# Kernel tuning notes

Hardware: AMD Instinct MI355X
Metric: run time of the kernel (lower is better)

The kernel has to match this reference:

```python
import jax, jax.numpy as jnp
import numpy as np
import math

B, S, D, H = 4, 2048, 1024, 16
DK = D // H  # 64


def setup_inputs() -> dict:
    key = jax.random.key(0)
    ks = jax.random.split(key, 10)
    scale = 1.0 / math.sqrt(D)
    inp = {
        "context_sequence": jax.random.normal(ks[0], (B, S, D), dtype=jnp.float32),
        "value_sequence": jax.random.normal(ks[1], (B, S, D), dtype=jnp.float32),
        "mask": jax.random.randint(ks[2], (S, S), 0, 2, dtype=jnp.int32),
        # stacked per-head projection params: [H, D, DK] weights, [H, DK] biases
        "Wq": jax.random.uniform(ks[3], (H, D, DK), jnp.float32, -scale, scale),
        "bq": jnp.zeros((H, DK), jnp.float32),
        "Wk": jax.random.uniform(ks[4], (H, D, DK), jnp.float32, -scale, scale),
        "bk": jnp.zeros((H, DK), jnp.float32),
        "Wv": jax.random.uniform(ks[5], (H, D, DK), jnp.float32, -scale, scale),
        "bv": jnp.zeros((H, DK), jnp.float32),
        "Wo": jax.random.uniform(ks[6], (D, D), jnp.float32, -scale, scale),
        "bo": jnp.zeros((D,), jnp.float32),
    }
    return inp


def reference(context_sequence, value_sequence, mask, Wq, bq, Wk, bk, Wv, bv, Wo, bo):
    # per-head projections batched over heads: [B,H,S,DK]
    Q = jnp.einsum("bsd,hdk->bhsk", context_sequence, Wq) + bq[None, :, None, :]
    K = jnp.einsum("bsd,hdk->bhsk", context_sequence, Wk) + bk[None, :, None, :]
    V = jnp.einsum("bsd,hdk->bhsk", value_sequence, Wv) + bv[None, :, None, :]
    scores = jnp.einsum("bhsk,bhtk->bhst", Q, K) / math.sqrt(DK)
    scores = jnp.where(mask[None, None, :, :] == 1, jnp.float32(-1e9), scores)
    attn = jax.nn.softmax(scores, axis=-1)
    out = jnp.einsum("bhst,bhtk->bhsk", attn, V)  # [B,H,S,DK]
    concat = out.transpose(0, 2, 1, 3).reshape(B, S, D)  # heads concatenated
    # output projection (dropout is identity in eval mode)
    return concat @ Wo.T + bo
```

## Files before the change

### kernel.cpp

```cpp
#include <hip/hip_runtime.h>
#include <hip/hip_bf16.h>

#define DEVI __device__ __forceinline__

typedef __attribute__((ext_vector_type(8))) short bf16x8;
typedef __attribute__((ext_vector_type(4))) float f32x4;
typedef unsigned short u16;
typedef unsigned long long u64;


DEVI void async16(const void* g, const void* l) {
  __builtin_amdgcn_global_load_lds(
      (const __attribute__((address_space(1))) unsigned int*)g,
      (__attribute__((address_space(3))) unsigned int*)l, 16, 0, 0);
}

DEVI u16 f2bf(float x) {
  unsigned int u = __float_as_uint(x);
  return (u16)((u + 0x7fffu + ((u >> 16) & 1u)) >> 16);
}

DEVI float fast_exp2(float x) {
#if __has_builtin(__builtin_amdgcn_exp2f)
  return __builtin_amdgcn_exp2f(x);
#else
  return exp2f(x);
#endif
}


__global__ __launch_bounds__(256) void prep_kernel(
    const float* __restrict__ ctx, const float* __restrict__ val, const int* __restrict__ msk,
    const float* __restrict__ Wq, const float* __restrict__ Wk, const float* __restrict__ Wv,
    const float* __restrict__ Wo, const float* __restrict__ bq, const float* __restrict__ bk,
    u16* __restrict__ Xc, u16* __restrict__ Xv, u16* __restrict__ Wqt, u16* __restrict__ Wkt,
    u16* __restrict__ Wvt, u16* __restrict__ WoB, u64* __restrict__ mbits, float* __restrict__ bqk) {
  __shared__ float tile[64 * 69];
  const int blk = blockIdx.x, tid = threadIdx.x;
  if (blk < 16384) {
    const float* src = (blk < 8192) ? ctx : val;
    u16* dst = (blk < 8192) ? Xc : Xv;
    int i = (blk & 8191) * 256 + tid;
    float4 v = ((const float4*)src)[i];
    ushort4 o;
    o.x = f2bf(v.x); o.y = f2bf(v.y); o.z = f2bf(v.z); o.w = f2bf(v.w);
    ((ushort4*)dst)[i] = o;
  } else if (blk < 17408) {
    int i = (blk - 16384) * 256 + tid;
    float4 v = ((const float4*)Wo)[i];
    ushort4 o;
    o.x = f2bf(v.x); o.y = f2bf(v.y); o.z = f2bf(v.z); o.w = f2bf(v.w);
    ((ushort4*)WoB)[i] = o;
  } else if (blk < 18176) {
    int t = blk - 17408;
    int mat = t >> 8, r = t & 255, h = r >> 4, d0 = (r & 15) * 64;
    const float* Ws = (mat == 0) ? Wq : (mat == 1) ? Wk : Wv;
    u16* Wd = (mat == 0) ? Wqt : (mat == 1) ? Wkt : Wvt;
    const int dg = tid & 15, rg = tid >> 4;
#pragma unroll
    for (int i = 0; i < 4; i++) {
      int dr = rg + i * 16;
      float4 v = *(const float4*)&Ws[((size_t)(h * 1024 + d0 + dr)) * 64 + dg * 4];
      tile[dr * 69 + dg * 4 + 0] = v.x;
      tile[dr * 69 + dg * 4 + 1] = v.y;
      tile[dr * 69 + dg * 4 + 2] = v.z;
      tile[dr * 69 + dg * 4 + 3] = v.w;
    }
    __syncthreads();
#pragma unroll
    for (int i = 0; i < 4; i++) {
      int k = rg + i * 16;
      ushort4 o;
      o.x = f2bf(tile[(dg * 4 + 0) * 69 + k]);
      o.y = f2bf(tile[(dg * 4 + 1) * 69 + k]);
      o.z = f2bf(tile[(dg * 4 + 2) * 69 + k]);
      o.w = f2bf(tile[(dg * 4 + 3) * 69 + k]);
      *(ushort4*)&Wd[(size_t)(h * 64 + k) * 1024 + d0 + dg * 4] = o;
    }
  } else if (blk < 34560) {
    int gid = (blk - 18176) * 256 + tid;
    u64 bal = __ballot(msk[gid] == 1);
    if ((tid & 63) == 0) mbits[(size_t)((gid >> 6) & 31) * 2048 + (gid >> 11)] = bal;
  } else {
    int i = (blk - 34560) * 256 + tid;
    bqk[i] = (i < 1024) ? bq[i] : bk[i - 1024];
  }
}


__global__ __launch_bounds__(256) void qkv_gemm(const u16* __restrict__ Xc, const u16* __restrict__ Xv,
                                                const u16* __restrict__ Wqkt, const u16* __restrict__ Wvt,
                                                const float* __restrict__ bqk, const float* __restrict__ bvv,
                                                u16* __restrict__ QKb, u16* __restrict__ Vtg, float qscale) {
  __shared__ __align__(16) u16 As[128 * 32];
  __shared__ __align__(16) u16 Bs[128 * 32];
  const int tid = threadIdx.x;
  const int w = tid >> 6, lane = tid & 63, quad = lane >> 4, lc = lane & 15;
  const int K = 1024;
  const bool isV = blockIdx.y >= 16;
  const int m0 = blockIdx.x * 128;
  const int n0 = (isV ? (blockIdx.y - 16) : blockIdx.y) * 128;
  const u16* A  = isV ? Xv : Xc;
  const u16* Bt = isV ? Wvt : Wqkt;
  const float* bias = isV ? bvv : bqk;
  const int wrow = (w >> 1) * 64, wcol = (w & 1) * 64;
  const int srow = tid >> 2, sc = tid & 3;
  const u16* Ag = A + (size_t)(m0 + srow) * K + sc * 8;
  const u16* Bg = Bt + (size_t)(n0 + srow) * K + sc * 8;
  u16* Asw = As + w * 512;
  u16* Bsw = Bs + w * 512;

  f32x4 acc[4][4] = {};
  for (int k0 = 0; k0 < K; k0 += 32) {
    async16(Ag + k0, Asw);
    async16(Ag + k0 + (size_t)64 * K, Asw + 2048);
    async16(Bg + k0, Bsw);
    async16(Bg + k0 + (size_t)64 * K, Bsw + 2048);
    __syncthreads();
    bf16x8 af[4], bfr[4];
#pragma unroll
    for (int rt = 0; rt < 4; rt++) af[rt] = *(const bf16x8*)&As[(wrow + rt * 16 + lc) * 32 + quad * 8];
#pragma unroll
    for (int ct = 0; ct < 4; ct++) bfr[ct] = *(const bf16x8*)&Bs[(wcol + ct * 16 + lc) * 32 + quad * 8];
#pragma unroll
    for (int rt = 0; rt < 4; rt++)
#pragma unroll
      for (int ct = 0; ct < 4; ct++)
        acc[rt][ct] = __builtin_amdgcn_mfma_f32_16x16x32_bf16(af[rt], bfr[ct], acc[rt][ct], 0, 0, 0);
    __syncthreads();
  }
#pragma unroll
  for (int ct = 0; ct < 4; ct++) {
    int col = n0 + wcol + ct * 16 + lc;
    float bv = bias[col];
    float os = (!isV && col < 1024) ? qscale : 1.0f;
#pragma unroll
    for (int rt = 0; rt < 4; rt++) {
      if (isV) {
        int trow = m0 + wrow + rt * 16 + quad * 4;
        ushort4 pk;
        pk.x = f2bf(acc[rt][ct][0] + bv);
        pk.y = f2bf(acc[rt][ct][1] + bv);
        pk.z = f2bf(acc[rt][ct][2] + bv);
        pk.w = f2bf(acc[rt][ct][3] + bv);
        size_t off = ((size_t)(trow >> 11) * 1024 + col) * 2048 + (trow & 2047);
        *(ushort4*)(Vtg + off) = pk;
      } else {
#pragma unroll
        for (int r = 0; r < 4; r++) {
          int row = m0 + wrow + rt * 16 + quad * 4 + r;
          QKb[(size_t)row * 2048 + col] = f2bf((acc[rt][ct][r] + bv) * os);
        }
      }
    }
  }
}


__global__ __launch_bounds__(256, 4) void attn_kernel(const u16* __restrict__ QK, const u16* __restrict__ Vt,
                                                      const u64* __restrict__ mbits, u16* __restrict__ AO) {
  __shared__ __align__(16) u16 Ks[2][4096];
  __shared__ __align__(16) u16 Vs[2][4096];
  __shared__ __align__(16) u16 Ps[4096];
  const int S = 2048, D = 1024, QS = 2048;
  const int tid = threadIdx.x, w = tid >> 6, lane = tid & 63, quad = lane >> 4, lc = lane & 15;
  const int q0 = blockIdx.x * 128;
  const int b = blockIdx.y >> 4, h = blockIdx.y & 15;
  const size_t baseq = (size_t)b * S * QS + (size_t)h * 64;
  const size_t vbase = (size_t)blockIdx.y * 64 * S;
  const int sr = lane >> 3, gch = (lane & 7) ^ sr, lx = lc & 7;
  u16* Ksq = (u16*)Ks;

#pragma unroll
  for (int i = 0; i < 4; i++) {
    const u16* g = QK + baseq + (size_t)(q0 + w * 32 + i * 8 + sr) * QS + gch * 8;
    async16(g, Ksq + w * 2048 + i * 512);
  }
  const u16* Kg0 = QK + baseq + 1024 + (size_t)(w * 16 + sr) * QS + gch * 8;
  const u16* Vg0 = Vt + vbase + (size_t)(w * 16 + sr) * S + gch * 8;
  __syncthreads();

  bf16x8 aq[2][2];
#pragma unroll
  for (int s = 0; s < 2; s++)
#pragma unroll
    for (int ks = 0; ks < 2; ks++)
      aq[s][ks] = *(const bf16x8*)&Ksq[w * 2048 + (s * 16 + lc) * 64 + (((ks * 4 + quad) ^ lx) << 3)];
  __syncthreads();

  async16(Kg0, Ks[0] + w * 1024);
  async16(Kg0 + (size_t)8 * QS, Ks[0] + w * 1024 + 512);
  async16(Vg0, Vs[0] + w * 1024);
  async16(Vg0 + (size_t)8 * S, Vs[0] + w * 1024 + 512);

  const u64* mrow = mbits + (size_t)(q0 + w * 32 + quad * 4);

  bf16x8 ones;
#pragma unroll
  for (int j = 0; j < 8; j++) ones[j] = (short)0x3F80;

  f32x4 acco[2][4] = {};
  f32x4 accl[2] = {};

  for (int t0 = 0; t0 < S; t0 += 64) {
    const int cur = (t0 >> 6) & 1;
    __syncthreads();
    if (t0 + 64 < S) {
      const u16* Kg = Kg0 + (size_t)(t0 + 64) * QS;
      const u16* Vg = Vg0 + (t0 + 64);
      async16(Kg, Ks[cur ^ 1] + w * 1024);
      async16(Kg + (size_t)8 * QS, Ks[cur ^ 1] + w * 1024 + 512);
      async16(Vg, Vs[cur ^ 1] + w * 1024);
      async16(Vg + (size_t)8 * S, Vs[cur ^ 1] + w * 1024 + 512);
    }

    f32x4 sacc[2][4] = {};
#pragma unroll
    for (int ks = 0; ks < 2; ks++)
#pragma unroll
      for (int ct = 0; ct < 4; ct++) {
        bf16x8 bk = *(const bf16x8*)&Ks[cur][(ct * 16 + lc) * 64 + (((ks * 4 + quad) ^ lx) << 3)];
        sacc[0][ct] = __builtin_amdgcn_mfma_f32_16x16x32_bf16(aq[0][ks], bk, sacc[0][ct], 0, 0, 0);
        sacc[1][ct] = __builtin_amdgcn_mfma_f32_16x16x32_bf16(aq[1][ks], bk, sacc[1][ct], 0, 0, 0);
      }

#pragma unroll
    for (int s = 0; s < 2; s++) {
#pragma unroll
      for (int r = 0; r < 4; r++) {
        u64 word = mrow[(size_t)(t0 >> 6) * 2048 + s * 16 + r];
        u64 wsh = word >> lc;
        unsigned int lo = (unsigned int)wsh, hi = (unsigned int)(wsh >> 32);
        float p0 = fast_exp2((lo & 1u)       ? -1e4f : sacc[s][0][r]);
        float p1 = fast_exp2((lo & 0x10000u) ? -1e4f : sacc[s][1][r]);
        float p2 = fast_exp2((hi & 1u)       ? -1e4f : sacc[s][2][r]);
        float p3 = fast_exp2((hi & 0x10000u) ? -1e4f : sacc[s][3][r]);
        const int q = quad * 4 + r, qx = q & 7, lch = lc >> 3;
        const int pb = w * 1024 + q * 64 + lx;
        Ps[pb + (((0 + lch) ^ qx) << 3)] = (u16)(__float_as_uint(p0) >> 16);
        Ps[pb + (((2 + lch) ^ qx) << 3)] = (u16)(__float_as_uint(p1) >> 16);
        Ps[pb + (((4 + lch) ^ qx) << 3)] = (u16)(__float_as_uint(p2) >> 16);
        Ps[pb + (((6 + lch) ^ qx) << 3)] = (u16)(__float_as_uint(p3) >> 16);
      }
#pragma unroll
      for (int ks = 0; ks < 2; ks++) {
        bf16x8 ap = *(const bf16x8*)&Ps[w * 1024 + lc * 64 + (((ks * 4 + quad) ^ lx) << 3)];
#pragma unroll
        for (int ct = 0; ct < 4; ct++) {
          bf16x8 bv = *(const bf16x8*)&Vs[cur][(ct * 16 + lc) * 64 + (((ks * 4 + quad) ^ lx) << 3)];
          acco[s][ct] = __builtin_amdgcn_mfma_f32_16x16x32_bf16(ap, bv, acco[s][ct], 0, 0, 0);
        }
        accl[s] = __builtin_amdgcn_mfma_f32_16x16x32_bf16(ap, ones, accl[s], 0, 0, 0);
      }
    }
  }

#pragma unroll
  for (int s = 0; s < 2; s++)
#pragma unroll
    for (int r = 0; r < 4; r++) {
      float inv = 1.0f / accl[s][r];
      size_t row = (size_t)b * S + q0 + w * 32 + s * 16 + quad * 4 + r;
#pragma unroll
      for (int ct = 0; ct < 4; ct++)
        AO[row * D + h * 64 + ct * 16 + lc] = f2bf(acco[s][ct][r] * inv);
    }
}


__global__ __launch_bounds__(256) void out_gemm(const u16* __restrict__ A, const u16* __restrict__ Bt,
                                                const float* __restrict__ bias, float* __restrict__ C) {
  __shared__ __align__(16) u16 As[128 * 32];
  __shared__ __align__(16) u16 Bs[128 * 32];
  const int tid = threadIdx.x;
  const int w = tid >> 6, lane = tid & 63, quad = lane >> 4, lc = lane & 15;
  const int K = 1024, N = 1024;
  const int m0 = blockIdx.x * 128, n0 = blockIdx.y * 128;
  const int wrow = (w >> 1) * 64, wcol = (w & 1) * 64;
  const int srow = tid >> 2, sc = tid & 3;
  const u16* Ag = A + (size_t)(m0 + srow) * K + sc * 8;
  const u16* Bg = Bt + (size_t)(n0 + srow) * K + sc * 8;
  u16* Asw = As + w * 512;
  u16* Bsw = Bs + w * 512;

  f32x4 acc[4][4] = {};
  for (int k0 = 0; k0 < K; k0 += 32) {
    async16(Ag + k0, Asw);
    async16(Ag + k0 + (size_t)64 * K, Asw + 2048);
    async16(Bg + k0, Bsw);
    async16(Bg + k0 + (size_t)64 * K, Bsw + 2048);
    __syncthreads();
    bf16x8 af[4], bfr[4];
#pragma unroll
    for (int rt = 0; rt < 4; rt++) af[rt] = *(const bf16x8*)&As[(wrow + rt * 16 + lc) * 32 + quad * 8];
#pragma unroll
    for (int ct = 0; ct < 4; ct++) bfr[ct] = *(const bf16x8*)&Bs[(wcol + ct * 16 + lc) * 32 + quad * 8];
#pragma unroll
    for (int rt = 0; rt < 4; rt++)
#pragma unroll
      for (int ct = 0; ct < 4; ct++)
        acc[rt][ct] = __builtin_amdgcn_mfma_f32_16x16x32_bf16(af[rt], bfr[ct], acc[rt][ct], 0, 0, 0);
    __syncthreads();
  }
#pragma unroll
  for (int ct = 0; ct < 4; ct++) {
    int col = n0 + wcol + ct * 16 + lc;
    float bv = bias[col];
#pragma unroll
    for (int rt = 0; rt < 4; rt++)
#pragma unroll
      for (int r = 0; r < 4; r++) {
        int row = m0 + wrow + rt * 16 + quad * 4 + r;
        C[(size_t)row * N + col] = acc[rt][ct][r] + bv;
      }
  }
}


extern "C" void kernel_launch(void* const* d_in, const int* in_sizes, int n_in,
                              void* d_out, int out_size, void* d_ws, size_t ws_size,
                              hipStream_t stream) {
  const int B = 4, S = 2048, D = 1024;
  const float* ctx = (const float*)d_in[0];
  const float* val = (const float*)d_in[1];
  const int*   msk = (const int*)d_in[2];
  const float* Wq  = (const float*)d_in[3];
  const float* bq  = (const float*)d_in[4];
  const float* Wk  = (const float*)d_in[5];
  const float* bk  = (const float*)d_in[6];
  const float* Wv  = (const float*)d_in[7];
  const float* bv  = (const float*)d_in[8];
  const float* Wo  = (const float*)d_in[9];
  const float* bo  = (const float*)d_in[10];
  float* out = (float*)d_out;

  char* ws = (char*)d_ws;
  size_t off = 0;
  auto alloc = [&](size_t sz) { void* p = ws + off; off += (sz + 255) & ~255ULL; return p; };
  const size_t NTOK = (size_t)B * S * D;
  u16* Xc  = (u16*)alloc(NTOK * 2);
  u16* Xv  = (u16*)alloc(NTOK * 2);
  u16* Wqt = (u16*)alloc((size_t)D * D * 2);
  u16* Wkt = (u16*)alloc((size_t)D * D * 2);
  u16* Wvt = (u16*)alloc((size_t)D * D * 2);
  u16* WoB = (u16*)alloc((size_t)D * D * 2);
  u16* QKb = (u16*)alloc(NTOK * 4);
  u16* Vtg = (u16*)alloc(NTOK * 2);
  u64* mbits = (u64*)alloc((size_t)S * S / 8);
  float* bqk = (float*)alloc(2048 * 4);
  u16* AO = Xc;
  if (off > ws_size) return;

  const float qscale = 0.125f * 1.44269504088896f;

  prep_kernel<<<34568, 256, 0, stream>>>(ctx, val, msk, Wq, Wk, Wv, Wo, bq, bk,
                                         Xc, Xv, Wqt, Wkt, Wvt, WoB, mbits, bqk);

  qkv_gemm<<<dim3(B * S / 128, 24), 256, 0, stream>>>(Xc, Xv, Wqt, Wvt, bqk, bv, QKb, Vtg, qscale);

  attn_kernel<<<dim3(S / 128, B * 16), 256, 0, stream>>>(QKb, Vtg, mbits, AO);

  out_gemm<<<dim3(B * S / 128, D / 128), 256, 0, stream>>>(AO, WoB, bo, out);
}
```

Before: 367.6 us.

## Keep softmax probabilities in registers by transposing QK^T MFMA and permuting K rows

The QK^T MFMA operands are swapped so each lane holds scores in the layout the PV MFMA A-operand needs. K rows are loaded in a permuted order so the probabilities can be packed straight into bf16x8 registers, which removes the LDS round trip through the Ps buffer. Mask words are now loaded once per tile per lane rather than per row. MFMA sections are wrapped in s_setprio to favour the matrix issue. The risk is extra register pressure at 4 waves per SIMD, and a mistake in the permutation would silently corrupt the output.

```diff
diff --git a/kernel.cpp b/kernel.cpp
--- a/kernel.cpp
+++ b/kernel.cpp
@@ -25,6 +25,14 @@
   return __builtin_amdgcn_exp2f(x);
 #else
   return exp2f(x);
+#endif
+}
+
+DEVI unsigned pk_bf16(unsigned hi, unsigned lo) {
+#if __has_builtin(__builtin_amdgcn_perm)
+  return __builtin_amdgcn_perm(hi, lo, 0x07060302u);
+#else
+  return (hi & 0xffff0000u) | (lo >> 16);
 #endif
 }
 
@@ -161,7 +169,6 @@
                                                       const u64* __restrict__ mbits, u16* __restrict__ AO) {
   __shared__ __align__(16) u16 Ks[2][4096];
   __shared__ __align__(16) u16 Vs[2][4096];
-  __shared__ __align__(16) u16 Ps[4096];
   const int S = 2048, D = 1024, QS = 2048;
   const int tid = threadIdx.x, w = tid >> 6, lane = tid & 63, quad = lane >> 4, lc = lane & 15;
   const int q0 = blockIdx.x * 128;
@@ -176,7 +183,8 @@
     const u16* g = QK + baseq + (size_t)(q0 + w * 32 + i * 8 + sr) * QS + gch * 8;
     async16(g, Ksq + w * 2048 + i * 512);
   }
-  const u16* Kg0 = QK + baseq + 1024 + (size_t)(w * 16 + sr) * QS + gch * 8;
+  const int kperm = 32 * (w & 1) + 4 * (w >> 1) + 8 * (sr >> 2) + (sr & 3);
+  const u16* Kg0 = QK + baseq + 1024 + (size_t)kperm * QS + gch * 8;
   const u16* Vg0 = Vt + vbase + (size_t)(w * 16 + sr) * S + gch * 8;
   __syncthreads();
 
@@ -189,11 +197,11 @@
   __syncthreads();
 
   async16(Kg0, Ks[0] + w * 1024);
-  async16(Kg0 + (size_t)8 * QS, Ks[0] + w * 1024 + 512);
+  async16(Kg0 + (size_t)16 * QS, Ks[0] + w * 1024 + 512);
   async16(Vg0, Vs[0] + w * 1024);
   async16(Vg0 + (size_t)8 * S, Vs[0] + w * 1024 + 512);
 
-  const u64* mrow = mbits + (size_t)(q0 + w * 32 + quad * 4);
+  const u64* mptr = mbits + (size_t)(q0 + w * 32 + lc);
 
   bf16x8 ones;
 #pragma unroll
@@ -209,49 +217,63 @@
       const u16* Kg = Kg0 + (size_t)(t0 + 64) * QS;
       const u16* Vg = Vg0 + (t0 + 64);
       async16(Kg, Ks[cur ^ 1] + w * 1024);
-      async16(Kg + (size_t)8 * QS, Ks[cur ^ 1] + w * 1024 + 512);
+      async16(Kg + (size_t)16 * QS, Ks[cur ^ 1] + w * 1024 + 512);
       async16(Vg, Vs[cur ^ 1] + w * 1024);
       async16(Vg + (size_t)8 * S, Vs[cur ^ 1] + w * 1024 + 512);
     }
 
+    u64 mw0 = mptr[(size_t)(t0 >> 6) * 2048];
+    u64 mw1 = mptr[(size_t)(t0 >> 6) * 2048 + 16];
+
     f32x4 sacc[2][4] = {};
+    __builtin_amdgcn_s_setprio(1);
 #pragma unroll
     for (int ks = 0; ks < 2; ks++)
 #pragma unroll
       for (int ct = 0; ct < 4; ct++) {
         bf16x8 bk = *(const bf16x8*)&Ks[cur][(ct * 16 + lc) * 64 + (((ks * 4 + quad) ^ lx) << 3)];
-        sacc[0][ct] = __builtin_amdgcn_mfma_f32_16x16x32_bf16(aq[0][ks], bk, sacc[0][ct], 0, 0, 0);
-        sacc[1][ct] = __builtin_amdgcn_mfma_f32_16x16x32_bf16(aq[1][ks], bk, sacc[1][ct], 0, 0, 0);
-      }
+        sacc[0][ct] = __builtin_amdgcn_mfma_f32_16x16x32_bf16(bk, aq[0][ks], sacc[0][ct], 0, 0, 0);
+        sacc[1][ct] = __builtin_amdgcn_mfma_f32_16x16x32_bf16(bk, aq[1][ks], sacc[1][ct], 0, 0, 0);
+      }
+    __builtin_amdgcn_s_setprio(0);
 
 #pragma unroll
     for (int s = 0; s < 2; s++) {
-#pragma unroll
-      for (int r = 0; r < 4; r++) {
-        u64 word = mrow[(size_t)(t0 >> 6) * 2048 + s * 16 + r];
-        u64 wsh = word >> lc;
-        unsigned int lo = (unsigned int)wsh, hi = (unsigned int)(wsh >> 32);
-        float p0 = fast_exp2((lo & 1u)       ? -1e4f : sacc[s][0][r]);
-        float p1 = fast_exp2((lo & 0x10000u) ? -1e4f : sacc[s][1][r]);
-        float p2 = fast_exp2((hi & 1u)       ? -1e4f : sacc[s][2][r]);
-        float p3 = fast_exp2((hi & 0x10000u) ? -1e4f : sacc[s][3][r]);
-        const int q = quad * 4 + r, qx = q & 7, lch = lc >> 3;
-        const int pb = w * 1024 + q * 64 + lx;
-        Ps[pb + (((0 + lch) ^ qx) << 3)] = (u16)(__float_as_uint(p0) >> 16);
-        Ps[pb + (((2 + lch) ^ qx) << 3)] = (u16)(__float_as_uint(p1) >> 16);
-        Ps[pb + (((4 + lch) ^ qx) << 3)] = (u16)(__float_as_uint(p2) >> 16);
-        Ps[pb + (((6 + lch) ^ qx) << 3)] = (u16)(__float_as_uint(p3) >> 16);
-      }
-#pragma unroll
-      for (int ks = 0; ks < 2; ks++) {
-        bf16x8 ap = *(const bf16x8*)&Ps[w * 1024 + lc * 64 + (((ks * 4 + quad) ^ lx) << 3)];
-#pragma unroll
-        for (int ct = 0; ct < 4; ct++) {
-          bf16x8 bv = *(const bf16x8*)&Vs[cur][(ct * 16 + lc) * 64 + (((ks * 4 + quad) ^ lx) << 3)];
-          acco[s][ct] = __builtin_amdgcn_mfma_f32_16x16x32_bf16(ap, bv, acco[s][ct], 0, 0, 0);
-        }
-        accl[s] = __builtin_amdgcn_mfma_f32_16x16x32_bf16(ap, ones, accl[s], 0, 0, 0);
-      }
+      u64 wq = (s == 0 ? mw0 : mw1) >> (quad * 8);
+      unsigned lo = (unsigned)wq, hi = (unsigned)(wq >> 32);
+      unsigned pu[4][4];
+#pragma unroll
+      for (int ct = 0; ct < 4; ct++) {
+        unsigned bits = (ct & 1) ? hi : lo;
+        const int sh = (ct >> 1) * 4;
+#pragma unroll
+        for (int r = 0; r < 4; r++)
+          pu[ct][r] = __float_as_uint(fast_exp2(((bits >> (sh + r)) & 1u) ? -1e4f : sacc[s][ct][r]));
+      }
+      union { unsigned u[4]; bf16x8 v; } f0, f1;
+      f0.u[0] = pk_bf16(pu[0][1], pu[0][0]);
+      f0.u[1] = pk_bf16(pu[0][3], pu[0][2]);
+      f0.u[2] = pk_bf16(pu[2][1], pu[2][0]);
+      f0.u[3] = pk_bf16(pu[2][3], pu[2][2]);
+      f1.u[0] = pk_bf16(pu[1][1], pu[1][0]);
+      f1.u[1] = pk_bf16(pu[1][3], pu[1][2]);
+      f1.u[2] = pk_bf16(pu[3][1], pu[3][0]);
+      f1.u[3] = pk_bf16(pu[3][3], pu[3][2]);
+
+      __builtin_amdgcn_s_setprio(1);
+#pragma unroll
+      for (int ct = 0; ct < 4; ct++) {
+        bf16x8 bv = *(const bf16x8*)&Vs[cur][(ct * 16 + lc) * 64 + ((quad ^ lx) << 3)];
+        acco[s][ct] = __builtin_amdgcn_mfma_f32_16x16x32_bf16(f0.v, bv, acco[s][ct], 0, 0, 0);
+      }
+      accl[s] = __builtin_amdgcn_mfma_f32_16x16x32_bf16(f0.v, ones, accl[s], 0, 0, 0);
+#pragma unroll
+      for (int ct = 0; ct < 4; ct++) {
+        bf16x8 bv = *(const bf16x8*)&Vs[cur][(ct * 16 + lc) * 64 + (((4 + quad) ^ lx) << 3)];
+        acco[s][ct] = __builtin_amdgcn_mfma_f32_16x16x32_bf16(f1.v, bv, acco[s][ct], 0, 0, 0);
+      }
+      accl[s] = __builtin_amdgcn_mfma_f32_16x16x32_bf16(f1.v, ones, accl[s], 0, 0, 0);
+      __builtin_amdgcn_s_setprio(0);
     }
   }
 
```

Result: faster. 340.9 us (-7.3%).
